# Optimization experiments

Hardware: AMD Instinct MI355X
Metric: run time of the kernel (lower is better)

Reference implementation:

```python
import jax, jax.numpy as jnp
import numpy as np

N_NODES = 50000
N_EDGES = 800000
D_IN = 128
D_OUT = 128


def setup_inputs() -> dict:
    key = jax.random.key(0)
    ks = jax.random.split(key, 10)
    x = jax.random.normal(ks[0], (N_NODES, D_IN), dtype=jnp.float32)
    lp_rows = jax.random.randint(ks[1], (N_EDGES,), 0, N_NODES, dtype=jnp.int32)
    lp_cols = jax.random.randint(ks[2], (N_EDGES,), 0, N_NODES, dtype=jnp.int32)
    # low-pass operator: positive normalized-adjacency-like weights
    lp_vals = jax.random.uniform(ks[3], (N_EDGES,), dtype=jnp.float32) / 16.0
    hp_rows = jax.random.randint(ks[4], (N_EDGES,), 0, N_NODES, dtype=jnp.int32)
    hp_cols = jax.random.randint(ks[5], (N_EDGES,), 0, N_NODES, dtype=jnp.int32)
    # high-pass operator: signed (Laplacian-like) weights
    hp_vals = jax.random.normal(ks[6], (N_EDGES,), dtype=jnp.float32) / 16.0
    alpha_w = jax.random.normal(ks[7], (1, D_IN), dtype=jnp.float32) * 0.05
    alpha_b = jnp.zeros((1,), dtype=jnp.float32)
    W = jax.random.normal(ks[8], (D_OUT, D_IN), dtype=jnp.float32) * (1.0 / np.sqrt(D_IN))
    b = jnp.zeros((D_OUT,), dtype=jnp.float32)
    return {"x": x, "lp_rows": lp_rows, "lp_cols": lp_cols, "lp_vals": lp_vals,
            "hp_rows": hp_rows, "hp_cols": hp_cols, "hp_vals": hp_vals,
            "alpha_w": alpha_w, "alpha_b": alpha_b, "W": W, "b": b}


def _spmm(rows, cols, vals, x, n):
    # COO sparse-dense matmul: out[r] += vals[e] * x[cols[e]]
    return jax.ops.segment_sum(vals[:, None] * x[cols], rows, num_segments=n)


def reference(x, lp_rows, lp_cols, lp_vals, hp_rows, hp_cols, hp_vals,
              alpha_w, alpha_b, W, b):
    n = x.shape[0]
    # per-node mixing gate: alpha_i = sigmoid(x_i . theta + b)  -> [N, 1]
    alpha = jax.nn.sigmoid(x @ alpha_w.T + alpha_b)
    z_lp = _spmm(lp_rows, lp_cols, lp_vals, x, n)   # [N, D_IN]
    z_hp = _spmm(hp_rows, hp_cols, hp_vals, x, n)   # [N, D_IN]
    z_mix = alpha * z_lp + (1.0 - alpha) * z_hp
    out = jax.nn.relu(z_mix @ W.T + b)              # use_activation=True
    return out, alpha
```

## Files before the change

kernel.cpp:

```cpp
#include <hip/hip_runtime.h>

#define N_NODES_C 50000
#define N_EDGES_C 800000
#define N_EDGES2_C (2 * N_EDGES_C)
#define D 128
#define NSHARD 8
#define SCAP 16
#define OFCAP 4096

#define GNODES 64
#define GP 16
#define LDP 132
#define GRID ((N_NODES_C + GNODES - 1) / GNODES)
#define EPB ((N_EDGES2_C + GRID - 1) / GRID)

static __device__ __forceinline__ unsigned short f2bf(float f) {
  unsigned u = __float_as_uint(f);
  u += 0x7fff + ((u >> 16) & 1);
  return (unsigned short)(u >> 16);
}
static __device__ __forceinline__ float bf_lo(unsigned u) {
  return __uint_as_float(u << 16);
}
static __device__ __forceinline__ float bf_hi(unsigned u) {
  return __uint_as_float(u & 0xffff0000u);
}

static __device__ __forceinline__ int xcd_id() {
  int v;
  asm volatile("s_getreg_b32 %0, hwreg(HW_REG_XCC_ID, 0, 4)" : "=s"(v));
  return v & (NSHARD - 1);
}

__global__ __launch_bounds__(256) void alpha_kernel(
    const float* __restrict__ x,
    const float* __restrict__ aw,
    const float* __restrict__ ab,
    float* __restrict__ alpha_out,
    float* __restrict__ alpha_ws,
    int n) {
  int wave = (int)((blockIdx.x * blockDim.x + threadIdx.x) >> 6);
  int lane = threadIdx.x & 63;
  if (wave >= n) return;
  const float* xr = x + (size_t)wave * D;
  float s = xr[lane] * aw[lane] + xr[lane + 64] * aw[lane + 64];
  #pragma unroll
  for (int off = 32; off > 0; off >>= 1)
    s += __shfl_down(s, off);
  if (lane == 0) {
    float a = 1.0f / (1.0f + __expf(-(s + ab[0])));
    alpha_out[wave] = a;
    alpha_ws[wave] = a;
  }
}

__global__ __launch_bounds__(256) void gemm_fill_kernel(
    const float* __restrict__ x,
    const float* __restrict__ W,
    unsigned* __restrict__ y,
    const int* __restrict__ lp_rows, const int* __restrict__ lp_cols,
    const float* __restrict__ lp_vals,
    const int* __restrict__ hp_rows, const int* __restrict__ hp_cols,
    const float* __restrict__ hp_vals,
    const float* __restrict__ alpha,
    int* __restrict__ rcursor,
    unsigned* __restrict__ pairs,
    int* __restrict__ ofcnt,
    uint2* __restrict__ ofl,
    int n) {
  __shared__ float wt[D][LDP];
  __shared__ float zs[GP][LDP];

  int t = threadIdx.x;
  int node0 = blockIdx.x * GNODES;

  #pragma unroll
  for (int it = 0; it < 16; ++it) {
    int f = t + it * 256;
    int j = f >> 5;
    int k4 = f & 31;
    *(float4*)&wt[j][k4 * 4] = ((const float4*)W)[f];
  }

  int tj = t >> 3;
  int ns = t & 7;
  int j0 = tj * 2;

  for (int p = 0; p < 4; ++p) {
    int nb = node0 + p * GP;
    __syncthreads();
    #pragma unroll
    for (int it = 0; it < 2; ++it) {
      int f = t + it * 256;
      int r = f >> 5;
      int c4 = f & 31;
      int node = nb + r;
      float4 v = make_float4(0.f, 0.f, 0.f, 0.f);
      if (node < n) v = ((const float4*)(x + (size_t)node * D))[c4];
      *(float4*)&zs[r][c4 * 4] = v;
    }
    __syncthreads();

    float acc[2][4] = {};
    #pragma unroll 4
    for (int k = 0; k < D; k += 4) {
      float4 w0 = *(const float4*)&wt[j0][k];
      float4 w1 = *(const float4*)&wt[j0 + 1][k];
      float4 w2 = *(const float4*)&wt[j0 + 64][k];
      float4 w3 = *(const float4*)&wt[j0 + 65][k];
      float4 z0 = *(const float4*)&zs[ns * 2 + 0][k];
      float4 z1 = *(const float4*)&zs[ns * 2 + 1][k];
      acc[0][0] += z0.x * w0.x + z0.y * w0.y + z0.z * w0.z + z0.w * w0.w;
      acc[0][1] += z0.x * w1.x + z0.y * w1.y + z0.z * w1.z + z0.w * w1.w;
      acc[0][2] += z0.x * w2.x + z0.y * w2.y + z0.z * w2.z + z0.w * w2.w;
      acc[0][3] += z0.x * w3.x + z0.y * w3.y + z0.z * w3.z + z0.w * w3.w;
      acc[1][0] += z1.x * w0.x + z1.y * w0.y + z1.z * w0.z + z1.w * w0.w;
      acc[1][1] += z1.x * w1.x + z1.y * w1.y + z1.z * w1.z + z1.w * w1.w;
      acc[1][2] += z1.x * w2.x + z1.y * w2.y + z1.z * w2.z + z1.w * w2.w;
      acc[1][3] += z1.x * w3.x + z1.y * w3.y + z1.z * w3.z + z1.w * w3.w;
    }

    #pragma unroll
    for (int ii = 0; ii < 2; ++ii) {
      int node = nb + ns * 2 + ii;
      if (node < n) {
        uint2 o;
        o.x = (unsigned)f2bf(acc[ii][0]) | ((unsigned)f2bf(acc[ii][2]) << 16);
        o.y = (unsigned)f2bf(acc[ii][1]) | ((unsigned)f2bf(acc[ii][3]) << 16);
        *(uint2*)&y[(size_t)node * 64 + j0] = o;
      }
    }
  }

  int xcc = xcd_id();
  int e0 = blockIdx.x * EPB;
  int e1 = e0 + EPB;
  if (e1 > N_EDGES2_C) e1 = N_EDGES2_C;
  for (int e = e0 + t; e < e1; e += 256) {
    int r, c;
    float v;
    if (e < N_EDGES_C) {
      r = lp_rows[e];
      c = lp_cols[e];
      v = lp_vals[e] * alpha[r];
    } else {
      int i = e - N_EDGES_C;
      r = hp_rows[i];
      c = hp_cols[i];
      v = hp_vals[i] * (1.0f - alpha[r]);
    }
    int p = atomicAdd(&rcursor[xcc * N_NODES_C + r], 1);
    if (p < SCAP) {
      unsigned pk = (unsigned)c | ((unsigned)f2bf(v) << 16);
      pairs[((size_t)r << 7) + (xcc << 4) + p] = pk;
    } else {
      int q = atomicAdd(ofcnt, 1);
      if (q < OFCAP)
        ofl[q] = make_uint2(((unsigned)r << 16) | (unsigned)c,
                            (unsigned)__float_as_int(v));
    }
  }
}

__global__ __launch_bounds__(256) void gather_kernel(
    const int* __restrict__ rcursor,
    const unsigned* __restrict__ pairs,
    const unsigned* __restrict__ y,
    const float* __restrict__ bias,
    const int* __restrict__ ofcnt,
    const uint2* __restrict__ ofl,
    float* __restrict__ out) {
  int row = (int)((blockIdx.x * blockDim.x + threadIdx.x) >> 6);
  int lane = threadIdx.x & 63;
  if (row >= N_NODES_C) return;

  const unsigned* rp = pairs + ((size_t)row << 7);
  unsigned w0 = rp[lane];
  unsigned w1 = rp[64 + lane];

  float aL = 0.f, aH = 0.f;
  #pragma unroll
  for (int s = 0; s < NSHARD; ++s) {
    int ds = rcursor[(size_t)s * N_NODES_C + row];
    if (ds > SCAP) ds = SCAP;
    unsigned wsrc = (s < 4) ? w0 : w1;
    int base = (s & 3) << 4;
    int p = 0;
    for (; p + 1 < ds; p += 2) {
      unsigned pk0 = (unsigned)__shfl((int)wsrc, base + p);
      unsigned pk1 = (unsigned)__shfl((int)wsrc, base + p + 1);
      unsigned u0 = y[(size_t)(pk0 & 0xffffu) * 64 + lane];
      unsigned u1 = y[(size_t)(pk1 & 0xffffu) * 64 + lane];
      float v0 = bf_hi(pk0);
      float v1 = bf_hi(pk1);
      aL += v0 * bf_lo(u0) + v1 * bf_lo(u1);
      aH += v0 * bf_hi(u0) + v1 * bf_hi(u1);
    }
    if (p < ds) {
      unsigned pk = (unsigned)__shfl((int)wsrc, base + p);
      unsigned u = y[(size_t)(pk & 0xffffu) * 64 + lane];
      aL += bf_hi(pk) * bf_lo(u);
      aH += bf_hi(pk) * bf_hi(u);
    }
  }

  int nof = *ofcnt;
  if (nof > OFCAP) nof = OFCAP;
  for (int i = 0; i < nof; ++i) {
    uint2 o = ofl[i];
    if ((int)(o.x >> 16) == row) {
      unsigned u = y[(size_t)(o.x & 0xffffu) * 64 + lane];
      float v = __int_as_float((int)o.y);
      aL += v * bf_lo(u);
      aH += v * bf_hi(u);
    }
  }

  out[(size_t)row * D + lane] = fmaxf(aL + bias[lane], 0.0f);
  out[(size_t)row * D + lane + 64] = fmaxf(aH + bias[lane + 64], 0.0f);
}

extern "C" void kernel_launch(void* const* d_in, const int* in_sizes, int n_in,
                              void* d_out, int out_size, void* d_ws, size_t ws_size,
                              hipStream_t stream) {
  const float* x = (const float*)d_in[0];
  const int* lp_rows = (const int*)d_in[1];
  const int* lp_cols = (const int*)d_in[2];
  const float* lp_vals = (const float*)d_in[3];
  const int* hp_rows = (const int*)d_in[4];
  const int* hp_cols = (const int*)d_in[5];
  const float* hp_vals = (const float*)d_in[6];
  const float* alpha_w = (const float*)d_in[7];
  const float* alpha_b = (const float*)d_in[8];
  const float* W = (const float*)d_in[9];
  const float* bias = (const float*)d_in[10];

  float* out = (float*)d_out;
  float* alpha_out = out + (size_t)N_NODES_C * D;

  char* ws = (char*)d_ws;
  unsigned* y = (unsigned*)ws;   ws += (size_t)N_NODES_C * 64 * 4;
  float* alpha_ws = (float*)ws;  ws += 200192;
  int* rcursor = (int*)ws;       ws += (size_t)N_NODES_C * NSHARD * 4;
  int* ofcnt = (int*)ws;         ws += 256;
  uint2* ofl = (uint2*)ws;       ws += (size_t)OFCAP * 8;
  unsigned* pairs = (unsigned*)ws;
  ws += (size_t)N_NODES_C * NSHARD * SCAP * 4;

  hipMemsetAsync(rcursor, 0,
                 (size_t)N_NODES_C * NSHARD * sizeof(int) + 256, stream);

  alpha_kernel<<<(N_NODES_C + 3) / 4, 256, 0, stream>>>(
      x, alpha_w, alpha_b, alpha_out, alpha_ws, N_NODES_C);

  gemm_fill_kernel<<<GRID, 256, 0, stream>>>(
      x, W, y,
      lp_rows, lp_cols, lp_vals, hp_rows, hp_cols, hp_vals,
      alpha_ws, rcursor, pairs, ofcnt, ofl, N_NODES_C);

  gather_kernel<<<(N_NODES_C * 64 + 255) / 256, 256, 0, stream>>>(
      rcursor, pairs, (const unsigned*)y, bias, ofcnt, ofl, out);
}
```

Measured before the change: 306.3 us.

## Split gather rows across two waves and halve GEMM LDS weight tile

Each output row in the gather kernel is now handled by two waves, one per half of the XCD shards, and the partial sums are combined through shared memory. The goal is more memory-level parallelism per row and shorter serial shard loops. The GEMM stage now stages W in two 64-row halves, which halves its LDS footprint to raise occupancy, but x tiles are reloaded twice. The y layout changes so output columns come out interleaved as pairs, allowing a contiguous float2 store. The extra shared-memory reduction and barrier add overhead.

```diff
diff --git a/kernel.cpp b/kernel.cpp
--- a/kernel.cpp
+++ b/kernel.cpp
@@ -68,66 +68,63 @@
     int* __restrict__ ofcnt,
     uint2* __restrict__ ofl,
     int n) {
-  __shared__ float wt[D][LDP];
+  __shared__ float wt[64][LDP];
   __shared__ float zs[GP][LDP];
 
   int t = threadIdx.x;
   int node0 = blockIdx.x * GNODES;
 
-  #pragma unroll
-  for (int it = 0; it < 16; ++it) {
-    int f = t + it * 256;
-    int j = f >> 5;
-    int k4 = f & 31;
-    *(float4*)&wt[j][k4 * 4] = ((const float4*)W)[f];
-  }
-
   int tj = t >> 3;
   int ns = t & 7;
-  int j0 = tj * 2;
-
-  for (int p = 0; p < 4; ++p) {
-    int nb = node0 + p * GP;
+  int jl = tj * 2;
+
+  for (int jh = 0; jh < 2; ++jh) {
     __syncthreads();
     #pragma unroll
-    for (int it = 0; it < 2; ++it) {
+    for (int it = 0; it < 8; ++it) {
       int f = t + it * 256;
-      int r = f >> 5;
-      int c4 = f & 31;
-      int node = nb + r;
-      float4 v = make_float4(0.f, 0.f, 0.f, 0.f);
-      if (node < n) v = ((const float4*)(x + (size_t)node * D))[c4];
-      *(float4*)&zs[r][c4 * 4] = v;
-    }
-    __syncthreads();
-
-    float acc[2][4] = {};
-    #pragma unroll 4
-    for (int k = 0; k < D; k += 4) {
-      float4 w0 = *(const float4*)&wt[j0][k];
-      float4 w1 = *(const float4*)&wt[j0 + 1][k];
-      float4 w2 = *(const float4*)&wt[j0 + 64][k];
-      float4 w3 = *(const float4*)&wt[j0 + 65][k];
-      float4 z0 = *(const float4*)&zs[ns * 2 + 0][k];
-      float4 z1 = *(const float4*)&zs[ns * 2 + 1][k];
-      acc[0][0] += z0.x * w0.x + z0.y * w0.y + z0.z * w0.z + z0.w * w0.w;
-      acc[0][1] += z0.x * w1.x + z0.y * w1.y + z0.z * w1.z + z0.w * w1.w;
-      acc[0][2] += z0.x * w2.x + z0.y * w2.y + z0.z * w2.z + z0.w * w2.w;
-      acc[0][3] += z0.x * w3.x + z0.y * w3.y + z0.z * w3.z + z0.w * w3.w;
-      acc[1][0] += z1.x * w0.x + z1.y * w0.y + z1.z * w0.z + z1.w * w0.w;
-      acc[1][1] += z1.x * w1.x + z1.y * w1.y + z1.z * w1.z + z1.w * w1.w;
-      acc[1][2] += z1.x * w2.x + z1.y * w2.y + z1.z * w2.z + z1.w * w2.w;
-      acc[1][3] += z1.x * w3.x + z1.y * w3.y + z1.z * w3.z + z1.w * w3.w;
-    }
-
-    #pragma unroll
-    for (int ii = 0; ii < 2; ++ii) {
-      int node = nb + ns * 2 + ii;
-      if (node < n) {
-        uint2 o;
-        o.x = (unsigned)f2bf(acc[ii][0]) | ((unsigned)f2bf(acc[ii][2]) << 16);
-        o.y = (unsigned)f2bf(acc[ii][1]) | ((unsigned)f2bf(acc[ii][3]) << 16);
-        *(uint2*)&y[(size_t)node * 64 + j0] = o;
+      int j = f >> 5;
+      int k4 = f & 31;
+      *(float4*)&wt[j][k4 * 4] =
+          ((const float4*)W)[(size_t)(jh * 64 + j) * 32 + k4];
+    }
+
+    for (int p = 0; p < 4; ++p) {
+      int nb = node0 + p * GP;
+      __syncthreads();
+      #pragma unroll
+      for (int it = 0; it < 2; ++it) {
+        int f = t + it * 256;
+        int r = f >> 5;
+        int c4 = f & 31;
+        int node = nb + r;
+        float4 v = make_float4(0.f, 0.f, 0.f, 0.f);
+        if (node < n) v = ((const float4*)(x + (size_t)node * D))[c4];
+        *(float4*)&zs[r][c4 * 4] = v;
+      }
+      __syncthreads();
+
+      float acc[2][2] = {};
+      #pragma unroll 4
+      for (int k = 0; k < D; k += 4) {
+        float4 w0 = *(const float4*)&wt[jl][k];
+        float4 w1 = *(const float4*)&wt[jl + 1][k];
+        float4 z0 = *(const float4*)&zs[ns * 2 + 0][k];
+        float4 z1 = *(const float4*)&zs[ns * 2 + 1][k];
+        acc[0][0] += z0.x * w0.x + z0.y * w0.y + z0.z * w0.z + z0.w * w0.w;
+        acc[0][1] += z0.x * w1.x + z0.y * w1.y + z0.z * w1.z + z0.w * w1.w;
+        acc[1][0] += z1.x * w0.x + z1.y * w0.y + z1.z * w0.z + z1.w * w0.w;
+        acc[1][1] += z1.x * w1.x + z1.y * w1.y + z1.z * w1.z + z1.w * w1.w;
+      }
+
+      #pragma unroll
+      for (int ii = 0; ii < 2; ++ii) {
+        int node = nb + ns * 2 + ii;
+        if (node < n) {
+          unsigned o = (unsigned)f2bf(acc[ii][0]) |
+                       ((unsigned)f2bf(acc[ii][1]) << 16);
+          y[(size_t)node * 64 + jh * 32 + tj] = o;
+        }
       }
     }
   }
@@ -170,54 +167,69 @@
     const int* __restrict__ ofcnt,
     const uint2* __restrict__ ofl,
     float* __restrict__ out) {
-  int row = (int)((blockIdx.x * blockDim.x + threadIdx.x) >> 6);
-  int lane = threadIdx.x & 63;
-  if (row >= N_NODES_C) return;
-
-  const unsigned* rp = pairs + ((size_t)row << 7);
-  unsigned w0 = rp[lane];
-  unsigned w1 = rp[64 + lane];
+  __shared__ float2 part[4][64];
+  int t = threadIdx.x;
+  int w = t >> 6;
+  int lane = t & 63;
+  int row = blockIdx.x * 2 + (w >> 1);
+  int half = w & 1;
 
   float aL = 0.f, aH = 0.f;
-  #pragma unroll
-  for (int s = 0; s < NSHARD; ++s) {
-    int ds = rcursor[(size_t)s * N_NODES_C + row];
-    if (ds > SCAP) ds = SCAP;
-    unsigned wsrc = (s < 4) ? w0 : w1;
-    int base = (s & 3) << 4;
-    int p = 0;
-    for (; p + 1 < ds; p += 2) {
-      unsigned pk0 = (unsigned)__shfl((int)wsrc, base + p);
-      unsigned pk1 = (unsigned)__shfl((int)wsrc, base + p + 1);
-      unsigned u0 = y[(size_t)(pk0 & 0xffffu) * 64 + lane];
-      unsigned u1 = y[(size_t)(pk1 & 0xffffu) * 64 + lane];
-      float v0 = bf_hi(pk0);
-      float v1 = bf_hi(pk1);
-      aL += v0 * bf_lo(u0) + v1 * bf_lo(u1);
-      aH += v0 * bf_hi(u0) + v1 * bf_hi(u1);
-    }
-    if (p < ds) {
-      unsigned pk = (unsigned)__shfl((int)wsrc, base + p);
-      unsigned u = y[(size_t)(pk & 0xffffu) * 64 + lane];
-      aL += bf_hi(pk) * bf_lo(u);
-      aH += bf_hi(pk) * bf_hi(u);
-    }
-  }
-
-  int nof = *ofcnt;
-  if (nof > OFCAP) nof = OFCAP;
-  for (int i = 0; i < nof; ++i) {
-    uint2 o = ofl[i];
-    if ((int)(o.x >> 16) == row) {
-      unsigned u = y[(size_t)(o.x & 0xffffu) * 64 + lane];
-      float v = __int_as_float((int)o.y);
-      aL += v * bf_lo(u);
-      aH += v * bf_hi(u);
-    }
-  }
-
-  out[(size_t)row * D + lane] = fmaxf(aL + bias[lane], 0.0f);
-  out[(size_t)row * D + lane + 64] = fmaxf(aH + bias[lane + 64], 0.0f);
+  if (row < N_NODES_C) {
+    const unsigned* rp = pairs + ((size_t)row << 7) + (half << 6);
+    unsigned wsrc = rp[lane];
+
+    #pragma unroll
+    for (int sc = 0; sc < 4; ++sc) {
+      int s = half * 4 + sc;
+      int ds = rcursor[(size_t)s * N_NODES_C + row];
+      if (ds > SCAP) ds = SCAP;
+      int base = sc << 4;
+      int p = 0;
+      for (; p + 1 < ds; p += 2) {
+        unsigned pk0 = (unsigned)__shfl((int)wsrc, base + p);
+        unsigned pk1 = (unsigned)__shfl((int)wsrc, base + p + 1);
+        unsigned u0 = y[(size_t)(pk0 & 0xffffu) * 64 + lane];
+        unsigned u1 = y[(size_t)(pk1 & 0xffffu) * 64 + lane];
+        float v0 = bf_hi(pk0);
+        float v1 = bf_hi(pk1);
+        aL += v0 * bf_lo(u0) + v1 * bf_lo(u1);
+        aH += v0 * bf_hi(u0) + v1 * bf_hi(u1);
+      }
+      if (p < ds) {
+        unsigned pk = (unsigned)__shfl((int)wsrc, base + p);
+        unsigned u = y[(size_t)(pk & 0xffffu) * 64 + lane];
+        aL += bf_hi(pk) * bf_lo(u);
+        aH += bf_hi(pk) * bf_hi(u);
+      }
+    }
+
+    if (half == 0) {
+      int nof = *ofcnt;
+      if (nof > OFCAP) nof = OFCAP;
+      for (int i = 0; i < nof; ++i) {
+        uint2 o = ofl[i];
+        if ((int)(o.x >> 16) == row) {
+          unsigned u = y[(size_t)(o.x & 0xffffu) * 64 + lane];
+          float v = __int_as_float((int)o.y);
+          aL += v * bf_lo(u);
+          aH += v * bf_hi(u);
+        }
+      }
+    }
+  }
+  part[w][lane] = make_float2(aL, aH);
+  __syncthreads();
+
+  if (half == 0 && row < N_NODES_C) {
+    float2 a = part[w][lane];
+    float2 b = part[w + 1][lane];
+    float2 bv = *(const float2*)&bias[lane * 2];
+    float2 o;
+    o.x = fmaxf(a.x + b.x + bv.x, 0.0f);
+    o.y = fmaxf(a.y + b.y + bv.y, 0.0f);
+    *(float2*)&out[(size_t)row * D + lane * 2] = o;
+  }
 }
 
 extern "C" void kernel_launch(void* const* d_in, const int* in_sizes, int n_in,
@@ -258,6 +270,6 @@
       lp_rows, lp_cols, lp_vals, hp_rows, hp_cols, hp_vals,
       alpha_ws, rcursor, pairs, ofcnt, ofl, N_NODES_C);
 
-  gather_kernel<<<(N_NODES_C * 64 + 255) / 256, 256, 0, stream>>>(
+  gather_kernel<<<(N_NODES_C + 1) / 2, 256, 0, stream>>>(
       rcursor, pairs, (const unsigned*)y, bias, ofcnt, ofl, out);
 }
```

Measured after the change: 300.5 us. About the same (-1.9%).
